# Optimization experiments

Hardware: AMD Instinct MI355X
Metric: run time of the kernel (lower is better)

Reference implementation:

```python
import jax, jax.numpy as jnp
import numpy as np

B, H, W, D, K = 64, 32, 32, 128, 1024


def setup_inputs() -> dict:
    key = jax.random.key(0)
    k1, k2 = jax.random.split(key)
    z_e = jax.random.normal(k1, (B, H, W, D), dtype=jnp.float32)
    # GlorotUniform over (k, d): limit = sqrt(6 / (k + d))
    limit = float(np.sqrt(6.0 / (K + D)))
    codebook = jax.random.uniform(k2, (K, D), dtype=jnp.float32, minval=-limit, maxval=limit)
    return {"z_e": z_e, "codebook": codebook}


def reference(z_e, codebook):
    # Original: norm = ||z_e[..., None, :] - codebook||_2 over d, then argmin over k.
    # Squared distance has the same argmin; expand to avoid the (B,H,W,k,d) tensor:
    # ||z - c||^2 = ||z||^2 - 2 z.c + ||c||^2
    z2 = jnp.sum(z_e * z_e, axis=-1, keepdims=True)           # (B,H,W,1)
    c2 = jnp.sum(codebook * codebook, axis=-1)                # (k,)
    dots = jnp.einsum('bhwd,kd->bhwk', z_e, codebook)         # (B,H,W,k)
    dist2 = z2 - 2.0 * dots + c2                              # (B,H,W,k)
    q_z = jnp.argmin(dist2, axis=-1)                          # (B,H,W) int
    return q_z
```

## Files before the change

### kernel.cpp

```cpp
#include <hip/hip_runtime.h>
#include <stdint.h>

#define NPTS   65536
#define DDIM   128
#define KCODES 1024

typedef __attribute__((ext_vector_type(8))) _Float16  half8;
typedef __attribute__((ext_vector_type(4))) float     f32x4;
typedef __attribute__((ext_vector_type(4))) int       int4v;
typedef __attribute__((ext_vector_type(2))) _Float16  half2v;

__device__ __forceinline__ void split16(float x, _Float16& hi, _Float16& lo) {
  _Float16 h = (__builtin_fabsf(x) < 6.103515625e-05f) ? (_Float16)0.f : (_Float16)x;
  hi = h;
  lo = (_Float16)(__fmul_rn(__fsub_rn(x, (float)h), 2048.f));
}

__device__ __forceinline__ float np_sumsq_128(const float* __restrict__ row) {
  float r[8];
#pragma unroll
  for (int k = 0; k < 8; ++k) r[k] = __fmul_rn(row[k], row[k]);
  for (int i = 8; i < 128; i += 8)
#pragma unroll
    for (int k = 0; k < 8; ++k) r[k] = __fadd_rn(r[k], __fmul_rn(row[i + k], row[i + k]));
  float s01 = __fadd_rn(r[0], r[1]), s23 = __fadd_rn(r[2], r[3]);
  float s45 = __fadd_rn(r[4], r[5]), s67 = __fadd_rn(r[6], r[7]);
  return __fadd_rn(__fadd_rn(s01, s23), __fadd_rn(s45, s67));
}

__device__ __forceinline__ void async_copy16(const void* g, void* l) {
  auto gp = (const __attribute__((address_space(1))) unsigned int*)(uintptr_t)g;
  auto lp = (__attribute__((address_space(3))) unsigned int*)(unsigned)(uintptr_t)l;
  __builtin_amdgcn_global_load_lds(gp, lp, 16, 0, 0);
}

constexpr size_t SZ_B   = (size_t)KCODES * DDIM * 2;
constexpr size_t OFF_B1 = 0;
constexpr size_t OFF_B2 = SZ_B;
constexpr size_t OFF_C2 = 2 * SZ_B;
constexpr size_t WS_NEED = OFF_C2 + (size_t)KCODES * 4;

__global__ __launch_bounds__(256) void vq_prep_cb(const float* __restrict__ cb,
                                                  _Float16* __restrict__ B1,
                                                  _Float16* __restrict__ B2,
                                                  float* __restrict__ c2) {
  const int w = threadIdx.x >> 6, ln = threadIdx.x & 63;
  const int code = blockIdx.x * 4 + w;
  const float2 cv = ((const float2*)(cb + (size_t)code * DDIM))[ln];
  _Float16 h0, l0, h1, l1;
  split16(cv.x, h0, l0); split16(cv.y, h1, l1);
  const int kg = ln >> 2;
  const int o  = 2 * (ln & 3);
  const size_t dst = (size_t)code * DDIM + (size_t)((kg ^ (code & 15)) * 8 + o);
  *(half2v*)(B1 + dst) = (half2v){h0, h1};
  *(half2v*)(B2 + dst) = (half2v){l0, l1};

  if (threadIdx.x < 32) {
    const int cc = blockIdx.x * 4 + (threadIdx.x >> 3), jj = threadIdx.x & 7;
    const float* row = cb + (size_t)cc * DDIM;
    float e = row[jj];
    float acc = __fmul_rn(e, e);
    for (int i = 1; i < 16; ++i) {
      e = row[i * 8 + jj];
      acc = __fadd_rn(acc, __fmul_rn(e, e));
    }
    float a1 = __fadd_rn(acc, __shfl_xor(acc, 1));
    float a2 = __fadd_rn(a1, __shfl_xor(a1, 2));
    float a4 = __fadd_rn(a2, __shfl_xor(a2, 4));
    if (jj == 0) c2[cc] = a4;
  }
}

__global__ __launch_bounds__(256, 2) void vq_gemm(
    const float* __restrict__ z,
    const unsigned short* __restrict__ B1g, const unsigned short* __restrict__ B2g,
    const float* __restrict__ c2g, int* __restrict__ out) {
  __shared__ alignas(16) char smem[16384 + 16384 + 4096 + 512];
  unsigned short* Bs1 = (unsigned short*)smem;
  unsigned short* Bs2 = (unsigned short*)(smem + 16384);
  float* c2sh = (float*)(smem + 32768);
  float* z2sh = (float*)(smem + 32768 + 4096);
  float* Ls   = (float*)smem;

  const int tid = threadIdx.x;
  const int ln = tid & 63, wr = tid >> 6;
  const int l15 = ln & 15, q = ln >> 4;
  const size_t row0 = (size_t)blockIdx.x * 128;
  const float4* z4 = (const float4*)z;

  for (int cc = 0; cc < 4; ++cc) {
#pragma unroll
    for (int j = 0; j < 4; ++j) {
      const int idx = tid + j * 256;
      float4 v = z4[(row0 + cc * 32) * 32 + idx];
      *(float4*)&Ls[(idx >> 5) * 132 + (idx & 31) * 4] = v;
    }
    __syncthreads();
    {
      const int r = tid >> 3, jj = tid & 7;
      const float* row = &Ls[r * 132];
      float e = row[jj];
      float acc = __fmul_rn(e, e);
      for (int i = 1; i < 16; ++i) {
        e = row[i * 8 + jj];
        acc = __fadd_rn(acc, __fmul_rn(e, e));
      }
      float a1 = __fadd_rn(acc, __shfl_xor(acc, 1));
      float a2 = __fadd_rn(a1, __shfl_xor(a1, 2));
      float a4 = __fadd_rn(a2, __shfl_xor(a2, 4));
      if (jj == 0) z2sh[cc * 32 + r] = a4;
    }
    __syncthreads();
  }

#pragma unroll
  for (int j = 0; j < 4; ++j) {
    const int s = tid + j * 256;
    async_copy16(B2g + s * 8, Bs2 + s * 8);
    async_copy16(B1g + s * 8, Bs1 + s * 8);
  }
  async_copy16(c2g + tid * 4, c2sh + tid * 4);

  half8 a1f[2][4], a2f[2][4];
#pragma unroll
  for (int rf = 0; rf < 2; ++rf) {
    const float* zr = z + (row0 + wr * 32 + rf * 16 + l15) * DDIM;
#pragma unroll
    for (int ks = 0; ks < 4; ++ks) {
      float tmp[8];
      *(float4*)tmp       = *(const float4*)(zr + ks * 32 + q * 8);
      *(float4*)(tmp + 4) = *(const float4*)(zr + ks * 32 + q * 8 + 4);
      half8 h, l;
#pragma unroll
      for (int e = 0; e < 8; ++e) {
        _Float16 hh, ll;
        split16(tmp[e], hh, ll);
        h[e] = hh; l[e] = ll;
      }
      a1f[rf][ks] = h; a2f[rf][ks] = l;
    }
  }

  float mv[8];
  int mi[8];
#pragma unroll
  for (int i = 0; i < 8; ++i) { mv[i] = 3.0e38f; mi[i] = 0; }

  __syncthreads();

  float z2r[8];
#pragma unroll
  for (int rf = 0; rf < 2; ++rf)
#pragma unroll
    for (int reg = 0; reg < 4; ++reg)
      z2r[rf * 4 + reg] = z2sh[wr * 32 + rf * 16 + q * 4 + reg];

  f32x4 acc[2][4];

#pragma unroll
  for (int rf = 0; rf < 2; ++rf)
#pragma unroll
    for (int cf = 0; cf < 4; ++cf) acc[rf][cf] = (f32x4){0.f, 0.f, 0.f, 0.f};
#pragma unroll
  for (int ks = 0; ks < 4; ++ks) {
    half8 b[4];
#pragma unroll
    for (int cf = 0; cf < 4; ++cf)
      b[cf] = *(const half8*)&Bs2[(cf * 16 + l15) * 128 + (((ks * 4 + q) ^ l15) * 8)];
#pragma unroll
    for (int rf = 0; rf < 2; ++rf)
#pragma unroll
      for (int cf = 0; cf < 4; ++cf)
        acc[rf][cf] = __builtin_amdgcn_mfma_f32_16x16x32_f16(a1f[rf][ks], b[cf],
                                                             acc[rf][cf], 0, 0, 0);
  }

  for (int iter = 0; iter < 15; ++iter) {
    const int c0 = iter * 64;

    __syncthreads();
    {
#pragma unroll
      for (int j = 0; j < 4; ++j) {
        const int s = tid + j * 256;
        async_copy16(B2g + (size_t)(c0 + 64) * DDIM + s * 8, Bs2 + s * 8);
      }
    }

    half8 b1[4][4];
#pragma unroll
    for (int ks = 0; ks < 4; ++ks)
#pragma unroll
      for (int cf = 0; cf < 4; ++cf)
        b1[ks][cf] = *(const half8*)&Bs1[(cf * 16 + l15) * 128 + (((ks * 4 + q) ^ l15) * 8)];

#pragma unroll
    for (int ks = 0; ks < 4; ++ks)
#pragma unroll
      for (int rf = 0; rf < 2; ++rf)
#pragma unroll
        for (int cf = 0; cf < 4; ++cf)
          acc[rf][cf] = __builtin_amdgcn_mfma_f32_16x16x32_f16(a2f[rf][ks], b1[ks][cf],
                                                               acc[rf][cf], 0, 0, 0);
#pragma unroll
    for (int rf = 0; rf < 2; ++rf)
#pragma unroll
      for (int cf = 0; cf < 4; ++cf) acc[rf][cf] = acc[rf][cf] * 4.8828125e-4f;

#pragma unroll
    for (int ks = 0; ks < 4; ++ks)
#pragma unroll
      for (int rf = 0; rf < 2; ++rf)
#pragma unroll
        for (int cf = 0; cf < 4; ++cf)
          acc[rf][cf] = __builtin_amdgcn_mfma_f32_16x16x32_f16(a1f[rf][ks], b1[ks][cf],
                                                               acc[rf][cf], 0, 0, 0);

    float dsnap[2][4][4];
#pragma unroll
    for (int rf = 0; rf < 2; ++rf)
#pragma unroll
      for (int cf = 0; cf < 4; ++cf)
#pragma unroll
        for (int reg = 0; reg < 4; ++reg) dsnap[rf][cf][reg] = acc[rf][cf][reg];

    __syncthreads();
    {
#pragma unroll
      for (int j = 0; j < 4; ++j) {
        const int s = tid + j * 256;
        async_copy16(B1g + (size_t)(c0 + 64) * DDIM + s * 8, Bs1 + s * 8);
      }
    }

#pragma unroll
    for (int rf = 0; rf < 2; ++rf)
#pragma unroll
      for (int cf = 0; cf < 4; ++cf) acc[rf][cf] = (f32x4){0.f, 0.f, 0.f, 0.f};
#pragma unroll
    for (int ks = 0; ks < 4; ++ks) {
      half8 b[4];
#pragma unroll
      for (int cf = 0; cf < 4; ++cf)
        b[cf] = *(const half8*)&Bs2[(cf * 16 + l15) * 128 + (((ks * 4 + q) ^ l15) * 8)];
#pragma unroll
      for (int rf = 0; rf < 2; ++rf)
#pragma unroll
        for (int cf = 0; cf < 4; ++cf)
          acc[rf][cf] = __builtin_amdgcn_mfma_f32_16x16x32_f16(a1f[rf][ks], b[cf],
                                                               acc[rf][cf], 0, 0, 0);
    }

    {
      float c2v[4];
#pragma unroll
      for (int cf = 0; cf < 4; ++cf) c2v[cf] = c2sh[c0 + cf * 16 + l15];
#pragma unroll
      for (int rf = 0; rf < 2; ++rf)
#pragma unroll
        for (int reg = 0; reg < 4; ++reg) {
          const int slot = rf * 4 + reg;
          const float z2v = z2r[slot];
#pragma unroll
          for (int cf = 0; cf < 4; ++cf) {
            float dot = dsnap[rf][cf][reg];
            float v = __fadd_rn(__fsub_rn(z2v, __fmul_rn(2.f, dot)), c2v[cf]);
            int idx = c0 + cf * 16 + l15;
            if (v < mv[slot]) { mv[slot] = v; mi[slot] = idx; }
          }
        }
    }
  }

  {
    const int c0 = 960;
    __syncthreads();
    half8 b1[4][4];
#pragma unroll
    for (int ks = 0; ks < 4; ++ks)
#pragma unroll
      for (int cf = 0; cf < 4; ++cf)
        b1[ks][cf] = *(const half8*)&Bs1[(cf * 16 + l15) * 128 + (((ks * 4 + q) ^ l15) * 8)];
#pragma unroll
    for (int ks = 0; ks < 4; ++ks)
#pragma unroll
      for (int rf = 0; rf < 2; ++rf)
#pragma unroll
        for (int cf = 0; cf < 4; ++cf)
          acc[rf][cf] = __builtin_amdgcn_mfma_f32_16x16x32_f16(a2f[rf][ks], b1[ks][cf],
                                                               acc[rf][cf], 0, 0, 0);
#pragma unroll
    for (int rf = 0; rf < 2; ++rf)
#pragma unroll
      for (int cf = 0; cf < 4; ++cf) acc[rf][cf] = acc[rf][cf] * 4.8828125e-4f;
#pragma unroll
    for (int ks = 0; ks < 4; ++ks)
#pragma unroll
      for (int rf = 0; rf < 2; ++rf)
#pragma unroll
        for (int cf = 0; cf < 4; ++cf)
          acc[rf][cf] = __builtin_amdgcn_mfma_f32_16x16x32_f16(a1f[rf][ks], b1[ks][cf],
                                                               acc[rf][cf], 0, 0, 0);
    {
      float c2v[4];
#pragma unroll
      for (int cf = 0; cf < 4; ++cf) c2v[cf] = c2sh[c0 + cf * 16 + l15];
#pragma unroll
      for (int rf = 0; rf < 2; ++rf)
#pragma unroll
        for (int reg = 0; reg < 4; ++reg) {
          const int slot = rf * 4 + reg;
          const float z2v = z2r[slot];
#pragma unroll
          for (int cf = 0; cf < 4; ++cf) {
            float dot = acc[rf][cf][reg];
            float v = __fadd_rn(__fsub_rn(z2v, __fmul_rn(2.f, dot)), c2v[cf]);
            int idx = c0 + cf * 16 + l15;
            if (v < mv[slot]) { mv[slot] = v; mi[slot] = idx; }
          }
        }
    }
  }

#pragma unroll
  for (int slot = 0; slot < 8; ++slot) {
    float v = mv[slot];
    int i = mi[slot];
#pragma unroll
    for (int m = 1; m <= 8; m <<= 1) {
      float ov = __shfl_xor(v, m);
      int oi = __shfl_xor(i, m);
      if (ov < v || (ov == v && oi < i)) { v = ov; i = oi; }
    }
    mv[slot] = v; mi[slot] = i;
  }

  if (l15 == 0) {
#pragma unroll
    for (int rf = 0; rf < 2; ++rf) {
      int4v r = {mi[rf * 4 + 0], mi[rf * 4 + 1], mi[rf * 4 + 2], mi[rf * 4 + 3]};
      *(int4v*)&out[row0 + wr * 32 + rf * 16 + q * 4] = r;
    }
  }
}

__global__ __launch_bounds__(256) void vq_fallback(const float* __restrict__ z,
                                                   const float* __restrict__ cb,
                                                   int* __restrict__ out) {
  __shared__ float zs[DDIM];
  __shared__ float z2s;
  __shared__ float bv[256];
  __shared__ int bi[256];
  const int p = blockIdx.x, tid = threadIdx.x;
  if (tid < DDIM) zs[tid] = z[(size_t)p * DDIM + tid];
  __syncthreads();
  if (tid == 0) z2s = np_sumsq_128(zs);
  __syncthreads();
  const float z2p = z2s;
  float best = 3.0e38f;
  int bidx = 0;
  for (int c = tid; c < KCODES; c += 256) {
    const float* cr = cb + (size_t)c * DDIM;
    double acc = 0.0;
#pragma unroll 8
    for (int d = 0; d < DDIM; ++d) acc += (double)zs[d] * (double)cr[d];
    float dfl = (float)acc;
    float c2k = np_sumsq_128(cr);
    float v = __fadd_rn(__fsub_rn(z2p, __fmul_rn(2.f, dfl)), c2k);
    if (v < best) { best = v; bidx = c; }
  }
  bv[tid] = best; bi[tid] = bidx;
  __syncthreads();
  for (int off = 128; off > 0; off >>= 1) {
    if (tid < off) {
      if (bv[tid + off] < bv[tid] || (bv[tid + off] == bv[tid] && bi[tid + off] < bi[tid])) {
        bv[tid] = bv[tid + off]; bi[tid] = bi[tid + off];
      }
    }
    __syncthreads();
  }
  if (tid == 0) out[p] = bi[0];
}

extern "C" void kernel_launch(void* const* d_in, const int* in_sizes, int n_in,
                              void* d_out, int out_size, void* d_ws, size_t ws_size,
                              hipStream_t stream) {
  (void)in_sizes; (void)n_in; (void)out_size;
  const float* z = (const float*)d_in[0];
  const float* cb = (const float*)d_in[1];
  int* out = (int*)d_out;

  if (d_ws != nullptr && ws_size >= WS_NEED) {
    char* ws = (char*)d_ws;
    _Float16* B1 = (_Float16*)(ws + OFF_B1);
    _Float16* B2 = (_Float16*)(ws + OFF_B2);
    float* c2 = (float*)(ws + OFF_C2);

    vq_prep_cb<<<KCODES / 4, 256, 0, stream>>>(cb, B1, B2, c2);
    vq_gemm<<<NPTS / 128, 256, 0, stream>>>(
        z, (const unsigned short*)(ws + OFF_B1), (const unsigned short*)(ws + OFF_B2),
        c2, out);
  } else {
    vq_fallback<<<NPTS, 256, 0, stream>>>(z, cb, out);
  }
}
```

Baseline: 121.6 us.

## Restructure per-tile MFMA schedule with explicit vmcnt barriers and per-column B loads

```diff
diff --git a/kernel.cpp b/kernel.cpp
--- a/kernel.cpp
+++ b/kernel.cpp
@@ -155,88 +155,14 @@
     for (int reg = 0; reg < 4; ++reg)
       z2r[rf * 4 + reg] = z2sh[wr * 32 + rf * 16 + q * 4 + reg];
 
-  f32x4 acc[2][4];
-
-#pragma unroll
-  for (int rf = 0; rf < 2; ++rf)
-#pragma unroll
-    for (int cf = 0; cf < 4; ++cf) acc[rf][cf] = (f32x4){0.f, 0.f, 0.f, 0.f};
-#pragma unroll
-  for (int ks = 0; ks < 4; ++ks) {
-    half8 b[4];
-#pragma unroll
-    for (int cf = 0; cf < 4; ++cf)
-      b[cf] = *(const half8*)&Bs2[(cf * 16 + l15) * 128 + (((ks * 4 + q) ^ l15) * 8)];
-#pragma unroll
-    for (int rf = 0; rf < 2; ++rf)
-#pragma unroll
-      for (int cf = 0; cf < 4; ++cf)
-        acc[rf][cf] = __builtin_amdgcn_mfma_f32_16x16x32_f16(a1f[rf][ks], b[cf],
-                                                             acc[rf][cf], 0, 0, 0);
-  }
-
   for (int iter = 0; iter < 15; ++iter) {
     const int c0 = iter * 64;
-
-    __syncthreads();
-    {
-#pragma unroll
-      for (int j = 0; j < 4; ++j) {
-        const int s = tid + j * 256;
-        async_copy16(B2g + (size_t)(c0 + 64) * DDIM + s * 8, Bs2 + s * 8);
-      }
-    }
-
-    half8 b1[4][4];
-#pragma unroll
-    for (int ks = 0; ks < 4; ++ks)
-#pragma unroll
-      for (int cf = 0; cf < 4; ++cf)
-        b1[ks][cf] = *(const half8*)&Bs1[(cf * 16 + l15) * 128 + (((ks * 4 + q) ^ l15) * 8)];
-
-#pragma unroll
-    for (int ks = 0; ks < 4; ++ks)
-#pragma unroll
-      for (int rf = 0; rf < 2; ++rf)
-#pragma unroll
-        for (int cf = 0; cf < 4; ++cf)
-          acc[rf][cf] = __builtin_amdgcn_mfma_f32_16x16x32_f16(a2f[rf][ks], b1[ks][cf],
-                                                               acc[rf][cf], 0, 0, 0);
+    f32x4 acc[2][4];
 #pragma unroll
     for (int rf = 0; rf < 2; ++rf)
 #pragma unroll
-      for (int cf = 0; cf < 4; ++cf) acc[rf][cf] = acc[rf][cf] * 4.8828125e-4f;
-
-#pragma unroll
-    for (int ks = 0; ks < 4; ++ks)
-#pragma unroll
-      for (int rf = 0; rf < 2; ++rf)
-#pragma unroll
-        for (int cf = 0; cf < 4; ++cf)
-          acc[rf][cf] = __builtin_amdgcn_mfma_f32_16x16x32_f16(a1f[rf][ks], b1[ks][cf],
-                                                               acc[rf][cf], 0, 0, 0);
-
-    float dsnap[2][4][4];
-#pragma unroll
-    for (int rf = 0; rf < 2; ++rf)
-#pragma unroll
-      for (int cf = 0; cf < 4; ++cf)
-#pragma unroll
-        for (int reg = 0; reg < 4; ++reg) dsnap[rf][cf][reg] = acc[rf][cf][reg];
-
-    __syncthreads();
-    {
-#pragma unroll
-      for (int j = 0; j < 4; ++j) {
-        const int s = tid + j * 256;
-        async_copy16(B1g + (size_t)(c0 + 64) * DDIM + s * 8, Bs1 + s * 8);
-      }
-    }
-
-#pragma unroll
-    for (int rf = 0; rf < 2; ++rf)
-#pragma unroll
       for (int cf = 0; cf < 4; ++cf) acc[rf][cf] = (f32x4){0.f, 0.f, 0.f, 0.f};
+
 #pragma unroll
     for (int ks = 0; ks < 4; ++ks) {
       half8 b[4];
@@ -249,6 +175,54 @@
         for (int cf = 0; cf < 4; ++cf)
           acc[rf][cf] = __builtin_amdgcn_mfma_f32_16x16x32_f16(a1f[rf][ks], b[cf],
                                                                acc[rf][cf], 0, 0, 0);
+    }
+
+    asm volatile("" ::: "memory");
+    __builtin_amdgcn_s_barrier();
+    asm volatile("" ::: "memory");
+
+#pragma unroll
+    for (int j = 0; j < 4; ++j) {
+      const int s = tid + j * 256;
+      async_copy16(B2g + (size_t)(c0 + 64) * DDIM + s * 8, Bs2 + s * 8);
+    }
+
+    asm volatile("s_waitcnt vmcnt(4)" ::: "memory");
+    __builtin_amdgcn_s_barrier();
+    asm volatile("" ::: "memory");
+
+#pragma unroll
+    for (int cf = 0; cf < 4; ++cf) {
+      half8 b1c[4];
+#pragma unroll
+      for (int ks = 0; ks < 4; ++ks) {
+        b1c[ks] = *(const half8*)&Bs1[(cf * 16 + l15) * 128 + (((ks * 4 + q) ^ l15) * 8)];
+        asm volatile("" : "+v"(b1c[ks]));
+      }
+#pragma unroll
+      for (int ks = 0; ks < 4; ++ks)
+#pragma unroll
+        for (int rf = 0; rf < 2; ++rf)
+          acc[rf][cf] = __builtin_amdgcn_mfma_f32_16x16x32_f16(a2f[rf][ks], b1c[ks],
+                                                               acc[rf][cf], 0, 0, 0);
+#pragma unroll
+      for (int rf = 0; rf < 2; ++rf) acc[rf][cf] = acc[rf][cf] * 4.8828125e-4f;
+#pragma unroll
+      for (int ks = 0; ks < 4; ++ks)
+#pragma unroll
+        for (int rf = 0; rf < 2; ++rf)
+          acc[rf][cf] = __builtin_amdgcn_mfma_f32_16x16x32_f16(a1f[rf][ks], b1c[ks],
+                                                               acc[rf][cf], 0, 0, 0);
+    }
+
+    asm volatile("s_waitcnt vmcnt(0)" ::: "memory");
+    __builtin_amdgcn_s_barrier();
+    asm volatile("" ::: "memory");
+
+#pragma unroll
+    for (int j = 0; j < 4; ++j) {
+      const int s = tid + j * 256;
+      async_copy16(B1g + (size_t)(c0 + 64) * DDIM + s * 8, Bs1 + s * 8);
     }
 
     {
@@ -263,7 +237,7 @@
           const float z2v = z2r[slot];
 #pragma unroll
           for (int cf = 0; cf < 4; ++cf) {
-            float dot = dsnap[rf][cf][reg];
+            float dot = acc[rf][cf][reg];
             float v = __fadd_rn(__fsub_rn(z2v, __fmul_rn(2.f, dot)), c2v[cf]);
             int idx = c0 + cf * 16 + l15;
             if (v < mv[slot]) { mv[slot] = v; mi[slot] = idx; }
@@ -274,33 +248,54 @@
 
   {
     const int c0 = 960;
-    __syncthreads();
-    half8 b1[4][4];
-#pragma unroll
-    for (int ks = 0; ks < 4; ++ks)
+    f32x4 acc[2][4];
+#pragma unroll
+    for (int rf = 0; rf < 2; ++rf)
+#pragma unroll
+      for (int cf = 0; cf < 4; ++cf) acc[rf][cf] = (f32x4){0.f, 0.f, 0.f, 0.f};
+
+#pragma unroll
+    for (int ks = 0; ks < 4; ++ks) {
+      half8 b[4];
 #pragma unroll
       for (int cf = 0; cf < 4; ++cf)
-        b1[ks][cf] = *(const half8*)&Bs1[(cf * 16 + l15) * 128 + (((ks * 4 + q) ^ l15) * 8)];
-#pragma unroll
-    for (int ks = 0; ks < 4; ++ks)
+        b[cf] = *(const half8*)&Bs2[(cf * 16 + l15) * 128 + (((ks * 4 + q) ^ l15) * 8)];
 #pragma unroll
       for (int rf = 0; rf < 2; ++rf)
 #pragma unroll
         for (int cf = 0; cf < 4; ++cf)
-          acc[rf][cf] = __builtin_amdgcn_mfma_f32_16x16x32_f16(a2f[rf][ks], b1[ks][cf],
-                                                               acc[rf][cf], 0, 0, 0);
-#pragma unroll
-    for (int rf = 0; rf < 2; ++rf)
-#pragma unroll
-      for (int cf = 0; cf < 4; ++cf) acc[rf][cf] = acc[rf][cf] * 4.8828125e-4f;
-#pragma unroll
-    for (int ks = 0; ks < 4; ++ks)
-#pragma unroll
-      for (int rf = 0; rf < 2; ++rf)
-#pragma unroll
-        for (int cf = 0; cf < 4; ++cf)
-          acc[rf][cf] = __builtin_amdgcn_mfma_f32_16x16x32_f16(a1f[rf][ks], b1[ks][cf],
-                                                               acc[rf][cf], 0, 0, 0);
+          acc[rf][cf] = __builtin_amdgcn_mfma_f32_16x16x32_f16(a1f[rf][ks], b[cf],
+                                                               acc[rf][cf], 0, 0, 0);
+    }
+
+    asm volatile("s_waitcnt vmcnt(0)" ::: "memory");
+    __builtin_amdgcn_s_barrier();
+    asm volatile("" ::: "memory");
+
+#pragma unroll
+    for (int cf = 0; cf < 4; ++cf) {
+      half8 b1c[4];
+#pragma unroll
+      for (int ks = 0; ks < 4; ++ks) {
+        b1c[ks] = *(const half8*)&Bs1[(cf * 16 + l15) * 128 + (((ks * 4 + q) ^ l15) * 8)];
+        asm volatile("" : "+v"(b1c[ks]));
+      }
+#pragma unroll
+      for (int ks = 0; ks < 4; ++ks)
+#pragma unroll
+        for (int rf = 0; rf < 2; ++rf)
+          acc[rf][cf] = __builtin_amdgcn_mfma_f32_16x16x32_f16(a2f[rf][ks], b1c[ks],
+                                                               acc[rf][cf], 0, 0, 0);
+#pragma unroll
+      for (int rf = 0; rf < 2; ++rf) acc[rf][cf] = acc[rf][cf] * 4.8828125e-4f;
+#pragma unroll
+      for (int ks = 0; ks < 4; ++ks)
+#pragma unroll
+        for (int rf = 0; rf < 2; ++rf)
+          acc[rf][cf] = __builtin_amdgcn_mfma_f32_16x16x32_f16(a1f[rf][ks], b1c[ks],
+                                                               acc[rf][cf], 0, 0, 0);
+    }
+
     {
       float c2v[4];
 #pragma unroll
```

New measurement: 121.7 us. No clear change (+0.1%).
